# Kernel optimization log

Measured on AMD Instinct MI355X. Metric: run time of the kernel, lower is better.

The kernel has to match this reference:

```python
import jax, jax.numpy as jnp
from jax import lax
import numpy as np

K = 3  # kernel size per dim
P = 1  # padding per dim
DN = ('NCDHW', 'OIDHW', 'NCDHW')  # conv3d dimension numbers


def setup_inputs() -> dict:
    key = jax.random.key(0)
    k1, k2 = jax.random.split(key)
    x = jax.random.normal(k1, (2, 16, 24, 24, 24, 24), dtype=jnp.float32)
    # Full 4D kernel [out_c, in_c, k0, k1, k2, k3]; the torch module stores it as
    # k0 separate Conv3d layers with weights W[:, :, i] each.
    W = jax.random.normal(k2, (32, 16, K, K, K, K), dtype=jnp.float32) * 0.05
    return {"x": x, "W": W}


def _conv4d(x, W):
    # x: [b, c_in, D0, D1, D2, D3]; W: [c_out, c_in, K, K, K, K]
    # 'same' 4D conv (stride 1, pad 1, k 3), decomposed over the leading
    # kernel dim into K conv3d calls (same math as the torch module, where
    # frame_results[j - i] += Conv3d_i(x_padded[:, :, j]) ).
    b, c, D0, D1, D2, D3 = x.shape
    c_out = W.shape[0]
    xp = jnp.pad(x, ((0, 0), (0, 0), (P, P), (P, P), (P, P), (P, P)))
    O0 = D0  # stride 1, pad 1, k 3 -> same size
    out = None
    for i in range(K):
        xs = xp[:, :, i:i + O0]                               # [b,c,O0,D1+2,D2+2,D3+2]
        xs = xs.transpose(0, 2, 1, 3, 4, 5).reshape(
            b * O0, c, D1 + 2 * P, D2 + 2 * P, D3 + 2 * P)    # fold frame dim into batch
        o = lax.conv_general_dilated(xs, W[:, :, i], (1, 1, 1), 'VALID',
                                     dimension_numbers=DN)    # [b*O0, c_out, D1, D2, D3]
        o = o.reshape(b, O0, c_out, D1, D2, D3).transpose(0, 2, 1, 3, 4, 5)
        out = o if out is None else out + o
    return out


def reference(x, W):
    return _conv4d(x, W)
```

## Files before the change

kernel.cpp:

```cpp
#include <hip/hip_runtime.h>


#define D      24
#define D2_    (24*24)
#define D3_    (24*24*24)
#define D4_    (24*24*24*24)
#define CIN    16
#define COUT   32
#define TPW    3
#define NTHR   384
#define GRID   256
#define NTILES (2*24*24)

#define ROW_USH   (2*676*8)
#define WL_USH    (81*512)
#define LDS_BYTES ((WL_USH + 2*ROW_USH) * 2)

#define XT_ELEMS  (2*24*26*26*26*16)
#define XT_BYTES  (XT_ELEMS*2)
#define WT_ELEMS  (81*32*16)
#define CNT_OFF_B (XT_BYTES + WT_ELEMS*2)
#define WS_NEED   (CNT_OFF_B + 64)

typedef __bf16 bf16x8 __attribute__((ext_vector_type(8)));
typedef float  f32x16 __attribute__((ext_vector_type(16)));
typedef unsigned short ushort_t;
typedef ushort_t ushort8 __attribute__((ext_vector_type(8)));
typedef ushort_t ushort4_ __attribute__((ext_vector_type(4)));

union u2b8 { ushort8 u; bf16x8 b; };

typedef const __attribute__((address_space(1))) unsigned int gu32;
typedef __attribute__((address_space(3))) unsigned int lu32;

__device__ inline ushort_t f2bf(float f) {
    union { float f; unsigned u; } x; x.f = f;
    unsigned r = x.u + 0x7FFFu + ((x.u >> 16) & 1u);
    return (ushort_t)(r >> 16);
}

__device__ inline int fswz(int f) { return f ^ ((f >> 3) & 7); }

__global__ void __launch_bounds__(NTHR) conv4d_fused(
    const float* __restrict__ x,
    const float* __restrict__ W,
    float* __restrict__ out,
    ushort_t* __restrict__ ws)
{
    extern __shared__ __align__(16) ushort_t lds[];
    ushort_t* ldsW  = lds;
    ushort_t* slabs = lds + WL_USH;

    ushort_t* xt = ws;
    ushort_t* Wt = ws + XT_BYTES / 2;
    unsigned* cnt = (unsigned*)((char*)ws + CNT_OFF_B);

    const int bk  = blockIdx.x;
    const int tid = threadIdx.x;

    {
        const long gtid = (long)bk * NTHR + tid;
        const long nthr = (long)GRID * NTHR;
        for (long u = gtid; u < XT_ELEMS / 8; u += nthr) {
            const int pp = (int)(u % 676);
            long t2 = u / 676;
            const int h  = (int)(t2 & 1); t2 >>= 1;
            const int p1 = (int)(t2 % 26); t2 /= 26;
            const int d0 = (int)(t2 % 24);
            const int b  = (int)(t2 / 24);
            const int p2 = pp / 26, p3 = pp - 26 * (pp / 26);
            const int r1 = p1 - 1, r2 = p2 - 1, r3 = p3 - 1;
            ushort8 v;
            if ((unsigned)r1 < 24u && (unsigned)r2 < 24u && (unsigned)r3 < 24u) {
                const float* xp = x + (long)(b * 16 + h * 8) * D4_
                                    + d0 * D3_ + r1 * D2_ + r2 * D + r3;
                #pragma unroll
                for (int c = 0; c < 8; ++c) v[c] = f2bf(xp[(long)c * D4_]);
            } else {
                #pragma unroll
                for (int c = 0; c < 8; ++c) v[c] = 0;
            }
            *(ushort8*)&xt[u * 8] = v;
        }
        for (long i = gtid; i < WT_ELEMS; i += nthr) {
            const int tap = (int)(i >> 9);
            const int co  = (int)((i >> 4) & 31);
            const int ci  = (int)(i & 15);
            const int f   = fswz(co * 2 + (ci >> 3));
            Wt[tap * 512 + f * 8 + (ci & 7)] =
                f2bf(W[((long)co * 16 + ci) * 81 + tap]);
        }
    }

    __threadfence();
    __syncthreads();
    if (tid == 0) {
        __hip_atomic_fetch_add(cnt, 1u, __ATOMIC_ACQ_REL, __HIP_MEMORY_SCOPE_AGENT);
        while (__hip_atomic_load(cnt, __ATOMIC_ACQUIRE, __HIP_MEMORY_SCOPE_AGENT)
               < (unsigned)GRID)
            __builtin_amdgcn_s_sleep(2);
    }
    __syncthreads();

    const int lane = tid & 63;
    const int wave = tid >> 6;
    const int col  = lane & 31;
    const int hi   = lane >> 5;

    for (int c = wave; c < 81; c += 6)
        __builtin_amdgcn_global_load_lds(
            (gu32*)Wt + (c * 256 + lane * 4),
            (lu32*)(ldsW + c * 512), 16, 0, 0);

    const int afb = fswz(col * 2 + hi) * 8;

    int ppos[TPW], sbase[TPW];
    #pragma unroll
    for (int t = 0; t < TPW; ++t) {
        const int pos = (wave * TPW + t) * 32 + col;
        ppos[t]  = pos;
        sbase[t] = (hi * 676 + (pos / D) * 26 + (pos % D)) * 8;
    }

    const int xcd  = bk & 7;
    const int slot = bk >> 3;

    for (int t0 = slot; t0 < 144; t0 += 32) {
        const int tile = xcd * 144 + t0;
        const int b   = tile / 576;
        const int d01 = tile % 576;
        const int d0  = d01 / 24;
        const int d1  = d01 % 24;

        const int k0lo = (d0 == 0) ? 1 : 0;
        const int k0hi = (d0 == 23) ? 1 : 2;
        const int nb   = (k0hi - k0lo + 1) * 3;

        f32x16 acc[TPW];
        #pragma unroll
        for (int t = 0; t < TPW; ++t)
            #pragma unroll
            for (int r = 0; r < 16; ++r) acc[t][r] = 0.f;

        auto stage = [&](int i) {
            const int k0 = k0lo + i / 3, k1 = i - 3 * (i / 3);
            const int r0 = d0 + k0 - 1;
            const ushort_t* src = xt + ((long)(b * 24 + r0) * 26 + (d1 + k1))
                                       * (long)ROW_USH;
            ushort_t* dst = slabs + (i & 1) * ROW_USH;
            #pragma unroll
            for (int j = 0; j < 4; ++j) {
                const int c = wave + 6 * j;
                if (c < 22) {
                    const bool act = (c < 21) | (lane < 8);
                    if (act)
                        __builtin_amdgcn_global_load_lds(
                            (gu32*)src + (c * 256 + lane * 4),
                            (lu32*)(dst + c * 512), 16, 0, 0);
                }
            }
        };

        stage(0);
        for (int i = 0; i < nb; ++i) {
            __syncthreads();

            if (i + 1 < nb) stage(i + 1);

            const ushort_t* sbuf = slabs + (i & 1) * ROW_USH;
            const int k0 = k0lo + i / 3, k1 = i - 3 * (i / 3);

            const ushort_t* wl = ldsW + (long)(k0 * 27 + k1 * 9) * 512 + afb;
            bf16x8 af[9];
            #pragma unroll
            for (int kc = 0; kc < 9; ++kc) {
                u2b8 cvt; cvt.u = *(const ushort8*)(wl + kc * 512);
                af[kc] = cvt.b;
            }

            __builtin_amdgcn_s_setprio(1);
            #pragma unroll
            for (int kc = 0; kc < 9; ++kc) {
                const int ko = ((kc / 3) * 26 + (kc % 3)) * 8;
                #pragma unroll
                for (int t = 0; t < TPW; ++t) {
                    u2b8 cvt;
                    cvt.u = *(const ushort8*)&sbuf[sbase[t] + ko];
                    acc[t] = __builtin_amdgcn_mfma_f32_32x32x16_bf16(
                                 af[kc], cvt.b, acc[t], 0, 0, 0);
                }
            }
            __builtin_amdgcn_s_setprio(0);
        }

        float* ob = out + (long)b * COUT * D4_ + (long)d0 * D3_ + (long)d1 * D2_;
        #pragma unroll
        for (int t = 0; t < TPW; ++t) {
            #pragma unroll
            for (int r = 0; r < 16; ++r) {
                const int co = (r & 3) + 8 * (r >> 2) + 4 * hi;
                ob[(long)co * D4_ + ppos[t]] = acc[t][r];
            }
        }
        __syncthreads();
    }
}

__global__ __launch_bounds__(384) void conv4d_mfma_fb(
    const float* __restrict__ x,
    const float* __restrict__ W,
    float* __restrict__ out)
{
    __shared__ __align__(16) ushort_t slab[26 * 26 * CIN];
    __shared__ __align__(16) ushort_t agrp[9 * COUT * CIN];

    const int d01  = blockIdx.x;
    const int b    = blockIdx.y;
    const int d0   = d01 / D;
    const int d1   = d01 % D;
    const int tid  = threadIdx.x;
    const int lane = tid & 63;
    const int wave = tid >> 6;
    const int col  = lane & 31;
    const int hi   = lane >> 5;

    const int afbase = fswz(col * 2 + hi) * 8;
    int ppos[3], sbase[3];
    #pragma unroll
    for (int t = 0; t < 3; ++t) {
        int pos = (wave * 3 + t) * 32 + col;
        ppos[t]  = pos;
        sbase[t] = ((pos / D) * 26 + (pos % D)) * CIN + hi * 8;
    }

    f32x16 acc[3];
    #pragma unroll
    for (int t = 0; t < 3; ++t)
        #pragma unroll
        for (int r = 0; r < 16; ++r) acc[t][r] = 0.f;

    const float* xb = x + (long)b * CIN * D4_;

    for (int k0 = 0; k0 < 3; ++k0) {
        const int r0 = d0 + k0 - 1;
        if ((unsigned)r0 >= (unsigned)D) continue;
        for (int k1 = 0; k1 < 3; ++k1) {
            const int r1 = d1 + k1 - 1;
            if ((unsigned)r1 >= (unsigned)D) continue;

            __syncthreads();

            const float* xp = xb + (long)r0 * D3_ + (long)r1 * D2_;
            for (int idx = tid; idx < 26 * 26 * 2; idx += 384) {
                const int pidx = idx >> 1;
                const int h    = idx & 1;
                const int p2   = pidx / 26;
                const int p3   = pidx - p2 * 26;
                const int s2   = p2 - 1;
                const int s3   = p3 - 1;
                const bool in  = (unsigned)s2 < (unsigned)D &&
                                 (unsigned)s3 < (unsigned)D;
                const float* xs = xp + s2 * D + s3;
                ushort8 v;
                #pragma unroll
                for (int c = 0; c < 8; ++c) {
                    float f = in ? xs[(long)(h * 8 + c) * D4_] : 0.f;
                    v[c] = f2bf(f);
                }
                *(ushort8*)&slab[idx * 8] = v;
            }

            const int kw0 = k0 * 27 + k1 * 9;
            for (int u = tid; u < 9 * COUT * 4; u += 384) {
                const int tap = u >> 7;
                const int rem = u & 127;
                const int co  = rem >> 2;
                const int q   = rem & 3;
                const int ci0 = (q >> 1) * 8 + (q & 1) * 4;
                const float* wp = W + co * (CIN * 81) + kw0 + tap;
                ushort4_ v;
                #pragma unroll
                for (int c = 0; c < 4; ++c)
                    v[c] = f2bf(wp[(ci0 + c) * 81]);
                const int f  = co * 2 + (q >> 1);
                const int h2 = q & 1;
                *(ushort4_*)&agrp[tap * 512 + fswz(f) * 8 + h2 * 4] = v;
            }
            __syncthreads();

            bf16x8 af[9];
            #pragma unroll
            for (int kc = 0; kc < 9; ++kc) {
                u2b8 cvt;
                cvt.u = *(const ushort8*)&agrp[kc * 512 + afbase];
                af[kc] = cvt.b;
            }

            #pragma unroll
            for (int kc = 0; kc < 9; ++kc) {
                const int koff = ((kc / 3) * 26 + (kc % 3)) * CIN;
                #pragma unroll
                for (int t = 0; t < 3; ++t) {
                    u2b8 cvt;
                    cvt.u = *(const ushort8*)&slab[sbase[t] + koff];
                    acc[t] = __builtin_amdgcn_mfma_f32_32x32x16_bf16(
                                 af[kc], cvt.b, acc[t], 0, 0, 0);
                }
            }
        }
    }

    float* ob = out + (long)b * COUT * D4_ + (long)d0 * D3_ + (long)d1 * D2_;
    #pragma unroll
    for (int t = 0; t < 3; ++t) {
        #pragma unroll
        for (int r = 0; r < 16; ++r) {
            const int co = (r & 3) + 8 * (r >> 2) + 4 * hi;
            ob[(long)co * D4_ + ppos[t]] = acc[t][r];
        }
    }
}

extern "C" void kernel_launch(void* const* d_in, const int* in_sizes, int n_in,
                              void* d_out, int out_size, void* d_ws, size_t ws_size,
                              hipStream_t stream)
{
    const float* x = (const float*)d_in[0];
    const float* W = (const float*)d_in[1];
    float* out     = (float*)d_out;

    if (ws_size >= (size_t)WS_NEED) {
        hipFuncSetAttribute((const void*)conv4d_fused,
                            hipFuncAttributeMaxDynamicSharedMemorySize,
                            LDS_BYTES);
        hipMemsetAsync((char*)d_ws + CNT_OFF_B, 0, 64, stream);
        hipLaunchKernelGGL(conv4d_fused, dim3(GRID), dim3(NTHR), LDS_BYTES,
                           stream, x, W, out, (ushort_t*)d_ws);
    } else {
        hipLaunchKernelGGL(conv4d_mfma_fb, dim3(D * D, 2), dim3(384), 0, stream,
                           x, W, out);
    }
}
```

Baseline: 155.7 us.

## Compute two adjacent d1 output rows per tile to reuse staged input rows

Each block iteration now produces outputs for two neighbouring d1 positions, using two accumulator sets. It streams 4 input rows per k0 instead of 3, and each staged row feeds both outputs through shifted kernel taps. This is meant to cut global-to-LDS staging and barrier count per output by about a third. It also adds a minimum-blocks hint of 2 to launch bounds. The doubled accumulators raise register pressure and risk spills under that cap, and the coarser pairs (576 over 256 blocks) may worsen load balance.

```diff
diff --git a/kernel.cpp b/kernel.cpp
--- a/kernel.cpp
+++ b/kernel.cpp
@@ -10,7 +10,7 @@
 #define TPW    3
 #define NTHR   384
 #define GRID   256
-#define NTILES (2*24*24)
+#define NPAIRS (2*24*12)
 
 #define ROW_USH   (2*676*8)
 #define WL_USH    (81*512)
@@ -41,7 +41,7 @@
 
 __device__ inline int fswz(int f) { return f ^ ((f >> 3) & 7); }
 
-__global__ void __launch_bounds__(NTHR) conv4d_fused(
+__global__ void __launch_bounds__(NTHR, 2) conv4d_fused(
     const float* __restrict__ x,
     const float* __restrict__ W,
     float* __restrict__ out,
@@ -125,32 +125,33 @@
     const int xcd  = bk & 7;
     const int slot = bk >> 3;
 
-    for (int t0 = slot; t0 < 144; t0 += 32) {
-        const int tile = xcd * 144 + t0;
-        const int b   = tile / 576;
-        const int d01 = tile % 576;
-        const int d0  = d01 / 24;
-        const int d1  = d01 % 24;
+    for (int pr = slot; pr < 72; pr += 32) {
+        const int pair = xcd * 72 + pr;
+        const int b    = pair / 288;
+        const int rem  = pair % 288;
+        const int d0   = rem / 12;
+        const int d1   = (rem % 12) * 2;
 
         const int k0lo = (d0 == 0) ? 1 : 0;
         const int k0hi = (d0 == 23) ? 1 : 2;
-        const int nb   = (k0hi - k0lo + 1) * 3;
-
-        f32x16 acc[TPW];
+        const int nb0  = k0hi - k0lo + 1;
+        const int nrow = nb0 * 4;
+
+        f32x16 accA[TPW], accB[TPW];
         #pragma unroll
         for (int t = 0; t < TPW; ++t)
             #pragma unroll
-            for (int r = 0; r < 16; ++r) acc[t][r] = 0.f;
-
-        auto stage = [&](int i) {
-            const int k0 = k0lo + i / 3, k1 = i - 3 * (i / 3);
-            const int r0 = d0 + k0 - 1;
-            const ushort_t* src = xt + ((long)(b * 24 + r0) * 26 + (d1 + k1))
+            for (int r = 0; r < 16; ++r) { accA[t][r] = 0.f; accB[t][r] = 0.f; }
+
+        auto stage = [&](int rc) {
+            const int g = rc >> 2, j = rc & 3;
+            const int r0 = d0 + k0lo + g - 1;
+            const ushort_t* src = xt + ((long)(b * 24 + r0) * 26 + (d1 + j))
                                        * (long)ROW_USH;
-            ushort_t* dst = slabs + (i & 1) * ROW_USH;
-            #pragma unroll
-            for (int j = 0; j < 4; ++j) {
-                const int c = wave + 6 * j;
+            ushort_t* dst = slabs + (rc & 1) * ROW_USH;
+            #pragma unroll
+            for (int jj = 0; jj < 4; ++jj) {
+                const int c = wave + 6 * jj;
                 if (c < 22) {
                     const bool act = (c < 21) | (lane < 8);
                     if (act)
@@ -161,15 +162,7 @@
             }
         };
 
-        stage(0);
-        for (int i = 0; i < nb; ++i) {
-            __syncthreads();
-
-            if (i + 1 < nb) stage(i + 1);
-
-            const ushort_t* sbuf = slabs + (i & 1) * ROW_USH;
-            const int k0 = k0lo + i / 3, k1 = i - 3 * (i / 3);
-
+        auto combo = [&](const ushort_t* sbuf, int k0, int k1, f32x16* acc) {
             const ushort_t* wl = ldsW + (long)(k0 * 27 + k1 * 9) * 512 + afb;
             bf16x8 af[9];
             #pragma unroll
@@ -177,7 +170,6 @@
                 u2b8 cvt; cvt.u = *(const ushort8*)(wl + kc * 512);
                 af[kc] = cvt.b;
             }
-
             __builtin_amdgcn_s_setprio(1);
             #pragma unroll
             for (int kc = 0; kc < 9; ++kc) {
@@ -191,6 +183,20 @@
                 }
             }
             __builtin_amdgcn_s_setprio(0);
+        };
+
+        stage(0);
+        for (int rc = 0; rc < nrow; ++rc) {
+            __syncthreads();
+
+            if (rc + 1 < nrow) stage(rc + 1);
+
+            const ushort_t* sbuf = slabs + (rc & 1) * ROW_USH;
+            const int g = rc >> 2, j = rc & 3;
+            const int k0 = k0lo + g;
+
+            if (j <= 2) combo(sbuf, k0, j, accA);
+            if (j >= 1) combo(sbuf, k0, j - 1, accB);
         }
 
         float* ob = out + (long)b * COUT * D4_ + (long)d0 * D3_ + (long)d1 * D2_;
@@ -199,7 +205,8 @@
             #pragma unroll
             for (int r = 0; r < 16; ++r) {
                 const int co = (r & 3) + 8 * (r >> 2) + 4 * hi;
-                ob[(long)co * D4_ + ppos[t]] = acc[t][r];
+                ob[(long)co * D4_ + ppos[t]]       = accA[t][r];
+                ob[(long)co * D4_ + D2_ + ppos[t]] = accB[t][r];
             }
         }
         __syncthreads();
```

Result: slower. 160.2 us (+2.9%).
